# Optimization experiments

Hardware: AMD Instinct MI355X
Metric: run time of the kernel (lower is better)

Reference implementation:

```python
import jax, jax.numpy as jnp
import numpy as np

N_NODES = 100000
N_EDGES = 1600000
NUM_GRAPHS = 64
HID = 32
EPS = 1e-5


def _seg_max0(x, ids, num_segments):
    # segment max; segments with no entries become 0 (PyG-style identity)
    m = jax.ops.segment_max(x, ids, num_segments=num_segments)
    return jnp.where(jnp.isfinite(m), m, 0.0)


def _pointnet_layer(h, pos, src, dst, W1, b1, W2, b2):
    # message: mlp(cat([h_j, pos_j - pos_i])) ; aggregate: max at target i
    edge_feat = jnp.concatenate([h[src], pos[src] - pos[dst]], axis=-1)  # [E, C+3]
    m = jnp.maximum(edge_feat @ W1 + b1, 0.0) @ W2 + b2                  # [E, out]
    return _seg_max0(m, dst, N_NODES)                                    # [N, out]


def _batchnorm(x, gamma, beta):
    # training-mode BatchNorm1d: batch stats, biased variance
    mu = jnp.mean(x, axis=0)
    var = jnp.mean((x - mu) ** 2, axis=0)
    return (x - mu) * jax.lax.rsqrt(var + EPS) * gamma + beta


def setup_inputs() -> dict:
    key = jax.random.key(0)
    ks = jax.random.split(key, 16)
    pos = jax.random.normal(ks[0], (N_NODES, 3), dtype=jnp.float32)
    edge_index = jax.random.randint(ks[1], (2, N_EDGES), 0, N_NODES, dtype=jnp.int64)
    batch = jnp.sort(jax.random.randint(ks[2], (N_NODES,), 0, NUM_GRAPHS, dtype=jnp.int64))

    def lin(k, fan_in, fan_out):
        lim = 1.0 / np.sqrt(fan_in)
        kw, kb = jax.random.split(k)
        W = jax.random.uniform(kw, (fan_in, fan_out), jnp.float32, -lim, lim)
        b = jax.random.uniform(kb, (fan_out,), jnp.float32, -lim, lim)
        return W, b

    W1a, b1a = lin(ks[3], 3 + 3, HID)
    W2a, b2a = lin(ks[4], HID, HID)
    W1b, b1b = lin(ks[5], HID + 3, 2 * HID)
    W2b, b2b = lin(ks[6], 2 * HID, 2 * HID)
    Wc, bc = lin(ks[7], 2 * HID, 2)
    return {
        'pos': pos, 'edge_index': edge_index, 'batch': batch,
        'W1a': W1a, 'b1a': b1a, 'W2a': W2a, 'b2a': b2a,
        'g1': jnp.ones((HID,), jnp.float32), 'beta1': jnp.zeros((HID,), jnp.float32),
        'W1b': W1b, 'b1b': b1b, 'W2b': W2b, 'b2b': b2b,
        'g2': jnp.ones((2 * HID,), jnp.float32), 'beta2': jnp.zeros((2 * HID,), jnp.float32),
        'Wc': Wc, 'bc': bc,
    }


def reference(pos, edge_index, batch, W1a, b1a, W2a, b2a, g1, beta1,
              W1b, b1b, W2b, b2b, g2, beta2, Wc, bc):
    src, dst = edge_index[0], edge_index[1]  # source j -> target i
    h = _pointnet_layer(pos, pos, src, dst, W1a, b1a, W2a, b2a)   # [N, 32]
    h = jnp.maximum(_batchnorm(h, g1, beta1), 0.0)
    h = _pointnet_layer(h, pos, src, dst, W1b, b1b, W2b, b2b)     # [N, 64]
    h = jnp.maximum(_batchnorm(h, g2, beta2), 0.0)
    g = _seg_max0(h, batch, NUM_GRAPHS)                            # [G, 64]
    return g @ Wc + bc                                             # [G, 2]
```

## Files before the change

kernel.cpp:

```cpp
#include <hip/hip_runtime.h>

#define NN 100000
#define NE 1600000
#define NG 64
#define BSZ 131
#define NBUK 764
#define NMR 132
#define NBLK1 391
#define EPB 4096

typedef __attribute__((ext_vector_type(8))) short bf16x8;
typedef __attribute__((ext_vector_type(4))) float f32x4;

union AFrag { bf16x8 v; uint4 u; };

__device__ __forceinline__ bool finitef(float v) {
    return (__float_as_uint(v) & 0x7F800000u) != 0x7F800000u;
}
__device__ __forceinline__ unsigned short f2bf(float f) {
    unsigned int u = __float_as_uint(f);
    u += 0x7fffu + ((u >> 16) & 1u);
    return (unsigned short)(u >> 16);
}
__device__ __forceinline__ unsigned int cvtpk(float lo, float hi) {
    unsigned int r;
    asm("v_cvt_pk_bf16_f32 %0, %1, %2" : "=v"(r) : "v"(lo), "v"(hi));
    return r;
}
__device__ __forceinline__ float bflo(unsigned int q) { return __uint_as_float(q << 16); }
__device__ __forceinline__ float bfhi(unsigned int q) { return __uint_as_float(q & 0xffff0000u); }

__device__ __forceinline__ unsigned int enc(float f) {
    unsigned int u = __float_as_uint(f);
    return (u & 0x80000000u) ? ~u : (u | 0x80000000u);
}
__device__ __forceinline__ float dec(unsigned int k) {
    unsigned int u = (k & 0x80000000u) ? (k ^ 0x80000000u) : ~k;
    return __uint_as_float(u);
}

__global__ __launch_bounds__(256) void p1count(const int* __restrict__ dst,
                                               int* __restrict__ gmat) {
    __shared__ int h[NBUK];
    int tid = threadIdx.x;
    for (int i = tid; i < NBUK; i += 256) h[i] = 0;
    __syncthreads();
    int e0 = blockIdx.x * EPB;
    #pragma unroll
    for (int i = 0; i < 16; ++i) {
        int e = e0 + tid + i * 256;
        if (e < NE) atomicAdd(&h[dst[e] / BSZ], 1);
    }
    __syncthreads();
    for (int i = tid; i < NBUK; i += 256) gmat[blockIdx.x * NBUK + i] = h[i];
}

__global__ __launch_bounds__(512) void scanA(int* __restrict__ gmat, int* __restrict__ tot) {
    __shared__ int ls[512];
    int b = blockIdx.x, tid = threadIdx.x;
    int v = (tid < NBLK1) ? gmat[tid * NBUK + b] : 0;
    ls[tid] = v;
    __syncthreads();
    for (int o = 1; o < 512; o <<= 1) {
        int t = (tid >= o) ? ls[tid - o] : 0;
        __syncthreads();
        ls[tid] += t;
        __syncthreads();
    }
    if (tid < NBLK1) gmat[tid * NBUK + b] = ls[tid] - v;
    if (tid == 511) tot[b] = ls[511];
}

__global__ __launch_bounds__(1024) void scanB(const int* __restrict__ tot,
        int* __restrict__ base,
        unsigned int* __restrict__ gmax, unsigned int* __restrict__ gneg) {
    __shared__ int ls[1024];
    int tid = threadIdx.x;
    int v = (tid < NBUK) ? tot[tid] : 0;
    ls[tid] = v;
    __syncthreads();
    for (int o = 1; o < 1024; o <<= 1) {
        int t = (tid >= o) ? ls[tid - o] : 0;
        __syncthreads();
        ls[tid] += t;
        __syncthreads();
    }
    if (tid < NBUK) base[tid] = ls[tid] - v;
    if (tid == 1023) base[NBUK] = ls[1023];
    for (int i = tid; i < NG * 64; i += 1024) { gmax[i] = 0u; gneg[i] = 0u; }
}

__global__ __launch_bounds__(256) void p1scatter(const int* __restrict__ src,
        const int* __restrict__ dst, const int* __restrict__ gmat,
        const int* __restrict__ base, int2* __restrict__ sedge) {
    __shared__ int cur[NBUK];
    int tid = threadIdx.x;
    for (int i = tid; i < NBUK; i += 256) cur[i] = base[i] + gmat[blockIdx.x * NBUK + i];
    __syncthreads();
    int e0 = blockIdx.x * EPB;
    #pragma unroll
    for (int i = 0; i < 16; ++i) {
        int e = e0 + tid + i * 256;
        if (e < NE) {
            int d = dst[e];
            int p = atomicAdd(&cur[d / BSZ], 1);
            sedge[p] = make_int2(src[e], d);
        }
    }
}

__global__ __launch_bounds__(256) void uA_kernel(const float* __restrict__ pos,
        const float* __restrict__ W1, const float* __restrict__ b1,
        unsigned short* __restrict__ PA, unsigned short* __restrict__ QA) {
    __shared__ float sWp[96], sWq[96], sb[32];
    if (threadIdx.x < 96) {
        float wt = W1[96 + threadIdx.x];
        sWq[threadIdx.x] = wt;
        sWp[threadIdx.x] = W1[threadIdx.x] + wt;
    }
    if (threadIdx.x < 32) sb[threadIdx.x] = b1[threadIdx.x];
    __syncthreads();
    int n = blockIdx.x * 256 + threadIdx.x;
    if (n >= NN) return;
    float p0 = pos[n * 3 + 0], p1 = pos[n * 3 + 1], p2 = pos[n * 3 + 2];
    float P[32], Q[32];
    #pragma unroll
    for (int c = 0; c < 32; ++c) {
        P[c] = fmaf(p2, sWp[64 + c], fmaf(p1, sWp[32 + c], fmaf(p0, sWp[c], sb[c])));
        Q[c] = fmaf(p2, sWq[64 + c], fmaf(p1, sWq[32 + c], p0 * sWq[c]));
    }
    uint4* po = (uint4*)(PA + (size_t)n * 32);
    uint4* qo = (uint4*)(QA + (size_t)n * 32);
    #pragma unroll
    for (int q = 0; q < 4; ++q) {
        po[q] = make_uint4(cvtpk(P[8*q],P[8*q+1]), cvtpk(P[8*q+2],P[8*q+3]),
                           cvtpk(P[8*q+4],P[8*q+5]), cvtpk(P[8*q+6],P[8*q+7]));
        qo[q] = make_uint4(cvtpk(Q[8*q],Q[8*q+1]), cvtpk(Q[8*q+2],Q[8*q+3]),
                           cvtpk(Q[8*q+4],Q[8*q+5]), cvtpk(Q[8*q+6],Q[8*q+7]));
    }
}

__global__ __launch_bounds__(256) void uB_kernel(const unsigned int* __restrict__ accA,
        const float* __restrict__ ssA, const float* __restrict__ pos,
        const float* __restrict__ W1, const float* __restrict__ b1,
        unsigned short* __restrict__ PB, unsigned short* __restrict__ QB) {
    __shared__ float sW[32 * 64];
    __shared__ float sWt[3 * 64];
    __shared__ float sb[64];
    for (int i = threadIdx.x; i < 32 * 64; i += 256) sW[i] = W1[i];
    if (threadIdx.x < 192) sWt[threadIdx.x] = W1[32 * 64 + threadIdx.x];
    if (threadIdx.x < 64) sb[threadIdx.x] = b1[threadIdx.x];
    __syncthreads();
    int n = blockIdx.x * 256 + threadIdx.x;
    if (n >= NN) return;
    float h[32];
    const uint4* a4 = (const uint4*)(accA + (size_t)n * 32);
    #pragma unroll
    for (int q = 0; q < 8; ++q) {
        uint4 v = a4[q];
        unsigned int vv[4] = {v.x, v.y, v.z, v.w};
        #pragma unroll
        for (int r = 0; r < 4; ++r) {
            int c = 4 * q + r;
            float x = dec(vv[r]);
            x = finitef(x) ? x : 0.f;
            h[c] = fmaxf(fmaf(x, ssA[c], ssA[32 + c]), 0.f);
        }
    }
    float p0 = pos[n * 3 + 0], p1 = pos[n * 3 + 1], p2 = pos[n * 3 + 2];
    float Q[64], P[64];
    #pragma unroll
    for (int c = 0; c < 64; ++c) {
        Q[c] = fmaf(p2, sWt[128 + c], fmaf(p1, sWt[64 + c], p0 * sWt[c]));
        P[c] = Q[c] + sb[c];
    }
    #pragma unroll
    for (int k = 0; k < 32; ++k) {
        float x = h[k];
        #pragma unroll
        for (int c = 0; c < 64; ++c) P[c] = fmaf(x, sW[k * 64 + c], P[c]);
    }
    uint4* po = (uint4*)(PB + (size_t)n * 64);
    uint4* qo = (uint4*)(QB + (size_t)n * 64);
    #pragma unroll
    for (int q = 0; q < 8; ++q) {
        po[q] = make_uint4(cvtpk(P[8*q],P[8*q+1]), cvtpk(P[8*q+2],P[8*q+3]),
                           cvtpk(P[8*q+4],P[8*q+5]), cvtpk(P[8*q+6],P[8*q+7]));
        qo[q] = make_uint4(cvtpk(Q[8*q],Q[8*q+1]), cvtpk(Q[8*q+2],Q[8*q+3]),
                           cvtpk(Q[8*q+4],Q[8*q+5]), cvtpk(Q[8*q+6],Q[8*q+7]));
    }
}

__global__ __launch_bounds__(256, 3) void edgeA(
        const unsigned short* __restrict__ PA, const unsigned short* __restrict__ QA,
        const int2* __restrict__ sedge, const int* __restrict__ bbase,
        const float* __restrict__ W2, const float* __restrict__ b2,
        unsigned int* __restrict__ accA, float* __restrict__ partials) {
    __shared__ __align__(16) short w2f[2 * 64 * 8];
    __shared__ int2   sed[256];
    __shared__ uchar4 srow4[64];
    __shared__ unsigned int nm[NMR * 32];
    __shared__ float  psum[256], psq[256];

    const int tid = threadIdx.x;
    const int b   = blockIdx.x;
    const int nb0 = b * BSZ;
    const int lane = tid & 63, wv = tid >> 6;
    const int kg = (lane >> 4);
    unsigned char* srow = (unsigned char*)srow4;

    #pragma unroll
    for (int ii = 0; ii < 4; ++ii) {
        int i = tid + ii * 256;
        int j = i & 7, ln = (i >> 3) & 63, t = (i >> 9) & 1;
        int k = ((ln >> 4) & 3) * 8 + j, col = (ln & 15) + 16 * t;
        w2f[i] = (short)f2bf(W2[k * 32 + col]);
    }
    for (int i = tid; i < NMR * 32; i += 256) nm[i] = 0;
    __syncthreads();

    float b2v[2];
    #pragma unroll
    for (int t = 0; t < 2; ++t) b2v[t] = b2[(lane & 15) + 16 * t];

    const int bs = bbase[b], be = bbase[b + 1];
    for (int e0 = bs; e0 < be; e0 += 256) {
        int idx = e0 + tid;
        bool ok = idx < be;
        int2 ed = ok ? sedge[idx] : make_int2(nb0, nb0);
        sed[tid] = ed;
        srow[tid] = ok ? (unsigned char)(ed.y - nb0) : (unsigned char)255;

        AFrag af[4];
        #pragma unroll
        for (int g = 0; g < 4; ++g) {
            int E = wv * 64 + g * 16 + (lane & 15);
            int s = sed[E].x, dd = sed[E].y;
            uint4 Pq = *(const uint4*)&PA[(size_t)s * 32 + kg * 8];
            uint4 Qq = *(const uint4*)&QA[(size_t)dd * 32 + kg * 8];
            unsigned int pu[4] = {Pq.x, Pq.y, Pq.z, Pq.w};
            unsigned int qu[4] = {Qq.x, Qq.y, Qq.z, Qq.w};
            unsigned int outw[4];
            #pragma unroll
            for (int p = 0; p < 4; ++p) {
                float vlo = fmaxf(bflo(pu[p]) - bflo(qu[p]), 0.f);
                float vhi = fmaxf(bfhi(pu[p]) - bfhi(qu[p]), 0.f);
                outw[p] = cvtpk(vlo, vhi);
            }
            af[g].u = make_uint4(outw[0], outw[1], outw[2], outw[3]);
        }

        #pragma unroll
        for (int t = 0; t < 2; ++t) {
            bf16x8 bfr = *(const bf16x8*)&w2f[(t * 64 + lane) * 8];
            f32x4 acc[4];
            #pragma unroll
            for (int g = 0; g < 4; ++g) {
                f32x4 c = {b2v[t], b2v[t], b2v[t], b2v[t]};
                acc[g] = __builtin_amdgcn_mfma_f32_16x16x32_bf16(af[g].v, bfr, c, 0, 0, 0);
            }
            int ch = t * 16 + (lane & 15);
            #pragma unroll
            for (int g = 0; g < 4; ++g) {
                int eb = wv * 64 + g * 16 + kg * 4;
                uchar4 s4 = srow4[eb >> 2];
                unsigned char ss[4] = {s4.x, s4.y, s4.z, s4.w};
                #pragma unroll
                for (int r = 0; r < 4; ++r)
                    if (ss[r] != 255) atomicMax(&nm[(int)ss[r] * 32 + ch], enc(acc[g][r]));
            }
        }
    }

    __syncthreads();
    {
        int c = tid & 31, sub = tid >> 5;
        float s = 0.f, q = 0.f;
        for (int nl = sub; nl < BSZ; nl += 8) {
            int n = nb0 + nl;
            if (n >= NN) break;
            unsigned int k = nm[nl * 32 + c];
            accA[(size_t)n * 32 + c] = k;
            float v = dec(k);
            v = finitef(v) ? v : 0.f;
            s += v; q = fmaf(v, v, q);
        }
        psum[tid] = s; psq[tid] = q;
    }
    __syncthreads();
    if (tid < 128) { psum[tid] += psum[tid + 128]; psq[tid] += psq[tid + 128]; }
    __syncthreads();
    if (tid < 64)  { psum[tid] += psum[tid + 64];  psq[tid] += psq[tid + 64]; }
    __syncthreads();
    if (tid < 32) {
        float s = psum[tid] + psum[tid + 32];
        float q = psq[tid]  + psq[tid + 32];
        partials[b * 64 + tid]      = s;
        partials[b * 64 + 32 + tid] = q;
    }
}

__global__ __launch_bounds__(256, 3) void edgeB(
        const unsigned short* __restrict__ PB, const unsigned short* __restrict__ QB,
        const int2* __restrict__ sedge, const int* __restrict__ bbase,
        const int* __restrict__ batch,
        const float* __restrict__ W2, const float* __restrict__ b2,
        float* __restrict__ partials,
        unsigned int* __restrict__ gmax, unsigned int* __restrict__ gneg) {
    __shared__ __align__(16) short w2f[2 * 4 * 64 * 8];
    __shared__ int2   sed[256];
    __shared__ uchar4 srow4[64];
    __shared__ unsigned int nm[NMR * 64];
    __shared__ float  psum[256], psq[256];

    const int tid = threadIdx.x;
    const int b   = blockIdx.x;
    const int nb0 = b * BSZ;
    const int lane = tid & 63, wv = tid >> 6;
    const int kg = (lane >> 4);
    unsigned char* srow = (unsigned char*)srow4;

    #pragma unroll
    for (int ii = 0; ii < 16; ++ii) {
        int i = tid + ii * 256;
        int j = i & 7, ln = (i >> 3) & 63, t = (i >> 9) & 3, ks = (i >> 11) & 1;
        int k = ks * 32 + ((ln >> 4) & 3) * 8 + j, col = (ln & 15) + 16 * t;
        w2f[i] = (short)f2bf(W2[k * 64 + col]);
    }
    for (int i = tid; i < NMR * 64; i += 256) nm[i] = 0;
    __syncthreads();

    float b2v[4];
    #pragma unroll
    for (int t = 0; t < 4; ++t) b2v[t] = b2[(lane & 15) + 16 * t];

    const int bs = bbase[b], be = bbase[b + 1];
    for (int e0 = bs; e0 < be; e0 += 256) {
        int idx = e0 + tid;
        bool ok = idx < be;
        int2 ed = ok ? sedge[idx] : make_int2(nb0, nb0);
        sed[tid] = ed;
        srow[tid] = ok ? (unsigned char)(ed.y - nb0) : (unsigned char)255;

        AFrag af[4][2];
        #pragma unroll
        for (int g = 0; g < 4; ++g) {
            int E = wv * 64 + g * 16 + (lane & 15);
            int s = sed[E].x, dd = sed[E].y;
            #pragma unroll
            for (int ks = 0; ks < 2; ++ks) {
                uint4 Pq = *(const uint4*)&PB[(size_t)s * 64 + ks * 32 + kg * 8];
                uint4 Qq = *(const uint4*)&QB[(size_t)dd * 64 + ks * 32 + kg * 8];
                unsigned int pu[4] = {Pq.x, Pq.y, Pq.z, Pq.w};
                unsigned int qu[4] = {Qq.x, Qq.y, Qq.z, Qq.w};
                unsigned int outw[4];
                #pragma unroll
                for (int p = 0; p < 4; ++p) {
                    float vlo = fmaxf(bflo(pu[p]) - bflo(qu[p]), 0.f);
                    float vhi = fmaxf(bfhi(pu[p]) - bfhi(qu[p]), 0.f);
                    outw[p] = cvtpk(vlo, vhi);
                }
                af[g][ks].u = make_uint4(outw[0], outw[1], outw[2], outw[3]);
            }
        }

        #pragma unroll
        for (int t = 0; t < 4; ++t) {
            bf16x8 bf0 = *(const bf16x8*)&w2f[((0 * 4 + t) * 64 + lane) * 8];
            bf16x8 bf1 = *(const bf16x8*)&w2f[((1 * 4 + t) * 64 + lane) * 8];
            f32x4 acc[4];
            #pragma unroll
            for (int g = 0; g < 4; ++g) {
                f32x4 c = {b2v[t], b2v[t], b2v[t], b2v[t]};
                c = __builtin_amdgcn_mfma_f32_16x16x32_bf16(af[g][0].v, bf0, c, 0, 0, 0);
                acc[g] = __builtin_amdgcn_mfma_f32_16x16x32_bf16(af[g][1].v, bf1, c, 0, 0, 0);
            }
            int ch = t * 16 + (lane & 15);
            #pragma unroll
            for (int g = 0; g < 4; ++g) {
                int eb = wv * 64 + g * 16 + kg * 4;
                uchar4 s4 = srow4[eb >> 2];
                unsigned char ss[4] = {s4.x, s4.y, s4.z, s4.w};
                #pragma unroll
                for (int r = 0; r < 4; ++r)
                    if (ss[r] != 255) atomicMax(&nm[(int)ss[r] * 64 + ch], enc(acc[g][r]));
            }
        }
    }

    __syncthreads();
    {
        int c = tid & 63, sub = tid >> 6;
        float s = 0.f, q = 0.f;
        float rmax = 0.f, rneg = 0.f; int curg = -1;
        for (int nl = sub; nl < BSZ; nl += 4) {
            int n = nb0 + nl;
            if (n >= NN) break;
            float v = dec(nm[nl * 64 + c]);
            v = finitef(v) ? v : 0.f;
            s += v; q = fmaf(v, v, q);
            int g = batch[n];
            if (g != curg) {
                if (curg >= 0) {
                    atomicMax(&gmax[curg * 64 + c], enc(rmax));
                    atomicMax(&gneg[curg * 64 + c], enc(rneg));
                }
                curg = g; rmax = v; rneg = -v;
            } else {
                rmax = fmaxf(rmax, v); rneg = fmaxf(rneg, -v);
            }
        }
        if (curg >= 0) {
            atomicMax(&gmax[curg * 64 + c], enc(rmax));
            atomicMax(&gneg[curg * 64 + c], enc(rneg));
        }
        psum[tid] = s; psq[tid] = q;
    }
    __syncthreads();
    if (tid < 128) { psum[tid] += psum[tid + 128]; psq[tid] += psq[tid + 128]; }
    __syncthreads();
    if (tid < 64) {
        float s = psum[tid] + psum[tid + 64];
        float q = psq[tid]  + psq[tid + 64];
        partials[b * 128 + tid]      = s;
        partials[b * 128 + 64 + tid] = q;
    }
}

template <int C>
__global__ __launch_bounds__(1024) void bn_final(const float* __restrict__ partials, int nblocks,
                         const float* __restrict__ gamma, const float* __restrict__ beta,
                         float* __restrict__ ss) {
    __shared__ float lsum[1024], lsq[1024];
    const int NCH = 1024 / C;
    int tid = threadIdx.x;
    int c = tid & (C - 1);
    int chunk = tid / C;
    float s = 0.f, q = 0.f;
    for (int b = chunk; b < nblocks; b += NCH) {
        s += partials[b * 2 * C + c];
        q += partials[b * 2 * C + C + c];
    }
    lsum[chunk * C + c] = s; lsq[chunk * C + c] = q;
    __syncthreads();
    #pragma unroll
    for (int o = 512; o >= C; o >>= 1) {
        if (tid < o && o >= C) {
            lsum[tid] += lsum[tid + o];
            lsq[tid]  += lsq[tid + o];
        }
        __syncthreads();
    }
    if (tid < C) {
        float mu  = lsum[tid] / (float)NN;
        float var = fmaxf(lsq[tid] / (float)NN - mu * mu, 0.f);
        float inv = rsqrtf(var + 1e-5f);
        float sc  = gamma[tid] * inv;
        ss[tid]     = sc;
        ss[C + tid] = fmaf(-mu, sc, beta[tid]);
    }
}

__global__ void final_gemm(const unsigned int* __restrict__ gmax,
                           const unsigned int* __restrict__ gneg,
                           const float* __restrict__ ss, const float* __restrict__ Wc,
                           const float* __restrict__ bc, float* __restrict__ out) {
    int t = threadIdx.x;
    if (t >= NG * 2) return;
    int g = t >> 1, o = t & 1;
    float s = bc[o];
    for (int k = 0; k < 64; ++k) {
        float sc = ss[k], sh = ss[64 + k];
        float xm = dec(gmax[g * 64 + k]), xn = dec(gneg[g * 64 + k]);
        float x = (sc >= 0.f) ? xm : -xn;
        float v = finitef(x) ? fmaxf(fmaf(sc, x, sh), 0.f) : 0.f;
        s = fmaf(v, Wc[k * 2 + o], s);
    }
    out[t] = s;
}

extern "C" void kernel_launch(void* const* d_in, const int* in_sizes, int n_in,
                              void* d_out, int out_size, void* d_ws, size_t ws_size,
                              hipStream_t stream) {
    const float* pos   = (const float*)d_in[0];
    const int*   ei    = (const int*)d_in[1];
    const int*   batch = (const int*)d_in[2];
    const float* W1a = (const float*)d_in[3];
    const float* b1a = (const float*)d_in[4];
    const float* W2a = (const float*)d_in[5];
    const float* b2a = (const float*)d_in[6];
    const float* g1  = (const float*)d_in[7];
    const float* be1 = (const float*)d_in[8];
    const float* W1b = (const float*)d_in[9];
    const float* b1b = (const float*)d_in[10];
    const float* W2b = (const float*)d_in[11];
    const float* b2b = (const float*)d_in[12];
    const float* g2  = (const float*)d_in[13];
    const float* be2 = (const float*)d_in[14];
    const float* Wc  = (const float*)d_in[15];
    const float* bc  = (const float*)d_in[16];
    const int* srcp = ei;
    const int* dstp = ei + NE;

    char* base_p = (char*)d_ws;
    size_t ofs = 0;
    auto alloc = [&](size_t bytes) { char* p = base_p + ofs; ofs = (ofs + bytes + 255) & ~(size_t)255; return p; };
    int*   gmat  = (int*)alloc((size_t)NBLK1 * NBUK * 4);
    int*   tot   = (int*)alloc(NBUK * 4);
    int*   bbase = (int*)alloc((NBUK + 1) * 4);
    int2*  sedge = (int2*)alloc((size_t)NE * 8);
    unsigned short* PA = (unsigned short*)alloc((size_t)NN * 32 * 2);
    unsigned short* QA = (unsigned short*)alloc((size_t)NN * 32 * 2);
    unsigned short* PB = PA;
    unsigned short* QB = (unsigned short*)alloc((size_t)NN * 64 * 2);
    unsigned int* accA = (unsigned int*)alloc((size_t)NN * 32 * 4);
    float* partA = (float*)alloc((size_t)NBUK * 64 * 4);
    float* partB = (float*)alloc((size_t)NBUK * 128 * 4);
    float* ssA   = (float*)alloc(64 * 4);
    float* ssB   = (float*)alloc(128 * 4);
    unsigned int* gmax = (unsigned int*)alloc(NG * 64 * 4);
    unsigned int* gneg = (unsigned int*)alloc(NG * 64 * 4);

    p1count<<<NBLK1, 256, 0, stream>>>(dstp, gmat);
    scanA<<<NBUK, 512, 0, stream>>>(gmat, tot);
    scanB<<<1, 1024, 0, stream>>>(tot, bbase, gmax, gneg);
    p1scatter<<<NBLK1, 256, 0, stream>>>(srcp, dstp, gmat, bbase, sedge);

    uA_kernel<<<(NN + 255) / 256, 256, 0, stream>>>(pos, W1a, b1a, PA, QA);
    edgeA<<<NBUK, 256, 0, stream>>>(PA, QA, sedge, bbase, W2a, b2a, accA, partA);
    bn_final<32><<<1, 1024, 0, stream>>>(partA, NBUK, g1, be1, ssA);

    uB_kernel<<<(NN + 255) / 256, 256, 0, stream>>>(accA, ssA, pos, W1b, b1b, PB, QB);
    edgeB<<<NBUK, 256, 0, stream>>>(PB, QB, sedge, bbase, batch, W2b, b2b, partB, gmax, gneg);
    bn_final<64><<<1, 1024, 0, stream>>>(partB, NBUK, g2, be2, ssB);
    final_gemm<<<1, 128, 0, stream>>>(gmax, gneg, ssB, Wc, bc, (float*)d_out);
}
```

Before: 205.0 us.

## Pack edges into 32-bit src|row words, shrink buckets, use wave shuffles

Edges are now stored as one 32-bit word (source index in the low 20 bits, local row in the bucket above it) instead of an int2, which halves the scatter and read traffic. The bucket size drops from 131 to 98 nodes (1021 buckets), and the shared node-max table is transposed to channel-major with a stride of 99 to reduce bank conflicts. The edge kernels no longer stage edges and rows in LDS; they distribute them with wave shuffles and prefetch the next edge word. Launch bounds rise for more occupancy, at the cost of more buckets in the scan and count kernels and more shuffle instructions per edge.

```diff
diff --git a/kernel.cpp b/kernel.cpp
--- a/kernel.cpp
+++ b/kernel.cpp
@@ -3,9 +3,9 @@
 #define NN 100000
 #define NE 1600000
 #define NG 64
-#define BSZ 131
-#define NBUK 764
-#define NMR 132
+#define BSZ 98
+#define NBUK 1021
+#define SENTROW 127
 #define NBLK1 391
 #define EPB 4096
 
@@ -92,7 +92,7 @@
 
 __global__ __launch_bounds__(256) void p1scatter(const int* __restrict__ src,
         const int* __restrict__ dst, const int* __restrict__ gmat,
-        const int* __restrict__ base, int2* __restrict__ sedge) {
+        const int* __restrict__ base, int* __restrict__ sedge) {
     __shared__ int cur[NBUK];
     int tid = threadIdx.x;
     for (int i = tid; i < NBUK; i += 256) cur[i] = base[i] + gmat[blockIdx.x * NBUK + i];
@@ -103,8 +103,10 @@
         int e = e0 + tid + i * 256;
         if (e < NE) {
             int d = dst[e];
-            int p = atomicAdd(&cur[d / BSZ], 1);
-            sedge[p] = make_int2(src[e], d);
+            int buk = d / BSZ;
+            int row = d - buk * BSZ;
+            int p = atomicAdd(&cur[buk], 1);
+            sedge[p] = src[e] | (row << 20);
         }
     }
 }
@@ -191,23 +193,20 @@
     }
 }
 
-__global__ __launch_bounds__(256, 3) void edgeA(
+__global__ __launch_bounds__(256, 6) void edgeA(
         const unsigned short* __restrict__ PA, const unsigned short* __restrict__ QA,
-        const int2* __restrict__ sedge, const int* __restrict__ bbase,
+        const int* __restrict__ sedge, const int* __restrict__ bbase,
         const float* __restrict__ W2, const float* __restrict__ b2,
         unsigned int* __restrict__ accA, float* __restrict__ partials) {
     __shared__ __align__(16) short w2f[2 * 64 * 8];
-    __shared__ int2   sed[256];
-    __shared__ uchar4 srow4[64];
-    __shared__ unsigned int nm[NMR * 32];
-    __shared__ float  psum[256], psq[256];
+    __shared__ unsigned int nm[32 * 99];
+    __shared__ float psum[256], psq[256];
 
     const int tid = threadIdx.x;
     const int b   = blockIdx.x;
     const int nb0 = b * BSZ;
     const int lane = tid & 63, wv = tid >> 6;
-    const int kg = (lane >> 4);
-    unsigned char* srow = (unsigned char*)srow4;
+    const int kg = lane >> 4;
 
     #pragma unroll
     for (int ii = 0; ii < 4; ++ii) {
@@ -216,7 +215,7 @@
         int k = ((ln >> 4) & 3) * 8 + j, col = (ln & 15) + 16 * t;
         w2f[i] = (short)f2bf(W2[k * 32 + col]);
     }
-    for (int i = tid; i < NMR * 32; i += 256) nm[i] = 0;
+    for (int i = tid; i < 32 * 99; i += 256) nm[i] = 0;
     __syncthreads();
 
     float b2v[2];
@@ -224,20 +223,32 @@
     for (int t = 0; t < 2; ++t) b2v[t] = b2[(lane & 15) + 16 * t];
 
     const int bs = bbase[b], be = bbase[b + 1];
+    int idx = bs + wv * 64 + lane;
+    int myed = (idx < be) ? sedge[idx] : (SENTROW << 20);
     for (int e0 = bs; e0 < be; e0 += 256) {
-        int idx = e0 + tid;
-        bool ok = idx < be;
-        int2 ed = ok ? sedge[idx] : make_int2(nb0, nb0);
-        sed[tid] = ed;
-        srow[tid] = ok ? (unsigned char)(ed.y - nb0) : (unsigned char)255;
+        int nxt = (idx + 256 < be) ? sedge[idx + 256] : (SENTROW << 20);
+        idx += 256;
+
+        int edg[4]; unsigned int rw4[4];
+        #pragma unroll
+        for (int g = 0; g < 4; ++g) {
+            edg[g] = __shfl(myed, g * 16 + (lane & 15), 64);
+            unsigned int p = 0;
+            #pragma unroll
+            for (int r = 0; r < 4; ++r) {
+                int e2 = __shfl(myed, g * 16 + kg * 4 + r, 64);
+                p |= ((unsigned int)(e2 >> 20) & 0xFFu) << (8 * r);
+            }
+            rw4[g] = p;
+        }
 
         AFrag af[4];
         #pragma unroll
         for (int g = 0; g < 4; ++g) {
-            int E = wv * 64 + g * 16 + (lane & 15);
-            int s = sed[E].x, dd = sed[E].y;
+            int s = edg[g] & 0xFFFFF;
+            int rq = min(edg[g] >> 20, BSZ - 1);
             uint4 Pq = *(const uint4*)&PA[(size_t)s * 32 + kg * 8];
-            uint4 Qq = *(const uint4*)&QA[(size_t)dd * 32 + kg * 8];
+            uint4 Qq = *(const uint4*)&QA[(size_t)(nb0 + rq) * 32 + kg * 8];
             unsigned int pu[4] = {Pq.x, Pq.y, Pq.z, Pq.w};
             unsigned int qu[4] = {Qq.x, Qq.y, Qq.z, Qq.w};
             unsigned int outw[4];
@@ -253,23 +264,19 @@
         #pragma unroll
         for (int t = 0; t < 2; ++t) {
             bf16x8 bfr = *(const bf16x8*)&w2f[(t * 64 + lane) * 8];
-            f32x4 acc[4];
+            int ch = t * 16 + (lane & 15);
             #pragma unroll
             for (int g = 0; g < 4; ++g) {
                 f32x4 c = {b2v[t], b2v[t], b2v[t], b2v[t]};
-                acc[g] = __builtin_amdgcn_mfma_f32_16x16x32_bf16(af[g].v, bfr, c, 0, 0, 0);
-            }
-            int ch = t * 16 + (lane & 15);
-            #pragma unroll
-            for (int g = 0; g < 4; ++g) {
-                int eb = wv * 64 + g * 16 + kg * 4;
-                uchar4 s4 = srow4[eb >> 2];
-                unsigned char ss[4] = {s4.x, s4.y, s4.z, s4.w};
+                f32x4 acc = __builtin_amdgcn_mfma_f32_16x16x32_bf16(af[g].v, bfr, c, 0, 0, 0);
                 #pragma unroll
-                for (int r = 0; r < 4; ++r)
-                    if (ss[r] != 255) atomicMax(&nm[(int)ss[r] * 32 + ch], enc(acc[g][r]));
-            }
-        }
+                for (int r = 0; r < 4; ++r) {
+                    int rr = (rw4[g] >> (8 * r)) & 0xFF;
+                    if (rr < BSZ) atomicMax(&nm[ch * 99 + rr], enc(acc[r]));
+                }
+            }
+        }
+        myed = nxt;
     }
 
     __syncthreads();
@@ -279,7 +286,7 @@
         for (int nl = sub; nl < BSZ; nl += 8) {
             int n = nb0 + nl;
             if (n >= NN) break;
-            unsigned int k = nm[nl * 32 + c];
+            unsigned int k = nm[c * 99 + nl];
             accA[(size_t)n * 32 + c] = k;
             float v = dec(k);
             v = finitef(v) ? v : 0.f;
@@ -293,32 +300,27 @@
     if (tid < 64)  { psum[tid] += psum[tid + 64];  psq[tid] += psq[tid + 64]; }
     __syncthreads();
     if (tid < 32) {
-        float s = psum[tid] + psum[tid + 32];
-        float q = psq[tid]  + psq[tid + 32];
-        partials[b * 64 + tid]      = s;
-        partials[b * 64 + 32 + tid] = q;
-    }
-}
-
-__global__ __launch_bounds__(256, 3) void edgeB(
+        partials[b * 64 + tid]      = psum[tid] + psum[tid + 32];
+        partials[b * 64 + 32 + tid] = psq[tid]  + psq[tid + 32];
+    }
+}
+
+__global__ __launch_bounds__(256, 4) void edgeB(
         const unsigned short* __restrict__ PB, const unsigned short* __restrict__ QB,
-        const int2* __restrict__ sedge, const int* __restrict__ bbase,
+        const int* __restrict__ sedge, const int* __restrict__ bbase,
         const int* __restrict__ batch,
         const float* __restrict__ W2, const float* __restrict__ b2,
         float* __restrict__ partials,
         unsigned int* __restrict__ gmax, unsigned int* __restrict__ gneg) {
     __shared__ __align__(16) short w2f[2 * 4 * 64 * 8];
-    __shared__ int2   sed[256];
-    __shared__ uchar4 srow4[64];
-    __shared__ unsigned int nm[NMR * 64];
-    __shared__ float  psum[256], psq[256];
+    __shared__ unsigned int nm[64 * 99];
+    __shared__ float psum[256], psq[256];
 
     const int tid = threadIdx.x;
     const int b   = blockIdx.x;
     const int nb0 = b * BSZ;
     const int lane = tid & 63, wv = tid >> 6;
-    const int kg = (lane >> 4);
-    unsigned char* srow = (unsigned char*)srow4;
+    const int kg = lane >> 4;
 
     #pragma unroll
     for (int ii = 0; ii < 16; ++ii) {
@@ -327,7 +329,7 @@
         int k = ks * 32 + ((ln >> 4) & 3) * 8 + j, col = (ln & 15) + 16 * t;
         w2f[i] = (short)f2bf(W2[k * 64 + col]);
     }
-    for (int i = tid; i < NMR * 64; i += 256) nm[i] = 0;
+    for (int i = tid; i < 64 * 99; i += 256) nm[i] = 0;
     __syncthreads();
 
     float b2v[4];
@@ -335,22 +337,34 @@
     for (int t = 0; t < 4; ++t) b2v[t] = b2[(lane & 15) + 16 * t];
 
     const int bs = bbase[b], be = bbase[b + 1];
+    int idx = bs + wv * 64 + lane;
+    int myed = (idx < be) ? sedge[idx] : (SENTROW << 20);
     for (int e0 = bs; e0 < be; e0 += 256) {
-        int idx = e0 + tid;
-        bool ok = idx < be;
-        int2 ed = ok ? sedge[idx] : make_int2(nb0, nb0);
-        sed[tid] = ed;
-        srow[tid] = ok ? (unsigned char)(ed.y - nb0) : (unsigned char)255;
+        int nxt = (idx + 256 < be) ? sedge[idx + 256] : (SENTROW << 20);
+        idx += 256;
+
+        int edg[4]; unsigned int rw4[4];
+        #pragma unroll
+        for (int g = 0; g < 4; ++g) {
+            edg[g] = __shfl(myed, g * 16 + (lane & 15), 64);
+            unsigned int p = 0;
+            #pragma unroll
+            for (int r = 0; r < 4; ++r) {
+                int e2 = __shfl(myed, g * 16 + kg * 4 + r, 64);
+                p |= ((unsigned int)(e2 >> 20) & 0xFFu) << (8 * r);
+            }
+            rw4[g] = p;
+        }
 
         AFrag af[4][2];
         #pragma unroll
         for (int g = 0; g < 4; ++g) {
-            int E = wv * 64 + g * 16 + (lane & 15);
-            int s = sed[E].x, dd = sed[E].y;
+            int s = edg[g] & 0xFFFFF;
+            int rq = min(edg[g] >> 20, BSZ - 1);
             #pragma unroll
             for (int ks = 0; ks < 2; ++ks) {
                 uint4 Pq = *(const uint4*)&PB[(size_t)s * 64 + ks * 32 + kg * 8];
-                uint4 Qq = *(const uint4*)&QB[(size_t)dd * 64 + ks * 32 + kg * 8];
+                uint4 Qq = *(const uint4*)&QB[(size_t)(nb0 + rq) * 64 + ks * 32 + kg * 8];
                 unsigned int pu[4] = {Pq.x, Pq.y, Pq.z, Pq.w};
                 unsigned int qu[4] = {Qq.x, Qq.y, Qq.z, Qq.w};
                 unsigned int outw[4];
@@ -368,24 +382,20 @@
         for (int t = 0; t < 4; ++t) {
             bf16x8 bf0 = *(const bf16x8*)&w2f[((0 * 4 + t) * 64 + lane) * 8];
             bf16x8 bf1 = *(const bf16x8*)&w2f[((1 * 4 + t) * 64 + lane) * 8];
-            f32x4 acc[4];
+            int ch = t * 16 + (lane & 15);
             #pragma unroll
             for (int g = 0; g < 4; ++g) {
                 f32x4 c = {b2v[t], b2v[t], b2v[t], b2v[t]};
                 c = __builtin_amdgcn_mfma_f32_16x16x32_bf16(af[g][0].v, bf0, c, 0, 0, 0);
-                acc[g] = __builtin_amdgcn_mfma_f32_16x16x32_bf16(af[g][1].v, bf1, c, 0, 0, 0);
-            }
-            int ch = t * 16 + (lane & 15);
-            #pragma unroll
-            for (int g = 0; g < 4; ++g) {
-                int eb = wv * 64 + g * 16 + kg * 4;
-                uchar4 s4 = srow4[eb >> 2];
-                unsigned char ss[4] = {s4.x, s4.y, s4.z, s4.w};
+                f32x4 acc = __builtin_amdgcn_mfma_f32_16x16x32_bf16(af[g][1].v, bf1, c, 0, 0, 0);
                 #pragma unroll
-                for (int r = 0; r < 4; ++r)
-                    if (ss[r] != 255) atomicMax(&nm[(int)ss[r] * 64 + ch], enc(acc[g][r]));
-            }
-        }
+                for (int r = 0; r < 4; ++r) {
+                    int rr = (rw4[g] >> (8 * r)) & 0xFF;
+                    if (rr < BSZ) atomicMax(&nm[ch * 99 + rr], enc(acc[r]));
+                }
+            }
+        }
+        myed = nxt;
     }
 
     __syncthreads();
@@ -396,7 +406,7 @@
         for (int nl = sub; nl < BSZ; nl += 4) {
             int n = nb0 + nl;
             if (n >= NN) break;
-            float v = dec(nm[nl * 64 + c]);
+            float v = dec(nm[c * 99 + nl]);
             v = finitef(v) ? v : 0.f;
             s += v; q = fmaf(v, v, q);
             int g = batch[n];
@@ -420,10 +430,8 @@
     if (tid < 128) { psum[tid] += psum[tid + 128]; psq[tid] += psq[tid + 128]; }
     __syncthreads();
     if (tid < 64) {
-        float s = psum[tid] + psum[tid + 64];
-        float q = psq[tid]  + psq[tid + 64];
-        partials[b * 128 + tid]      = s;
-        partials[b * 128 + 64 + tid] = q;
+        partials[b * 128 + tid]      = psum[tid] + psum[tid + 64];
+        partials[b * 128 + 64 + tid] = psq[tid]  + psq[tid + 64];
     }
 }
 
@@ -508,7 +516,7 @@
     int*   gmat  = (int*)alloc((size_t)NBLK1 * NBUK * 4);
     int*   tot   = (int*)alloc(NBUK * 4);
     int*   bbase = (int*)alloc((NBUK + 1) * 4);
-    int2*  sedge = (int2*)alloc((size_t)NE * 8);
+    int*   sedge = (int*)alloc((size_t)NE * 4);
     unsigned short* PA = (unsigned short*)alloc((size_t)NN * 32 * 2);
     unsigned short* QA = (unsigned short*)alloc((size_t)NN * 32 * 2);
     unsigned short* PB = PA;
```

New measurement: 219.0 us. 6.8% more time.
